# Kernel optimization log

Hardware: AMD Instinct MI355X
Metric: run time of the kernel (lower is better)

The kernel has to match this reference:

```python
import jax, jax.numpy as jnp
import numpy as np

BATCH, SEQ, D_IN, D_OUT = 32, 1024, 128, 128
NEG_SLOPE = 0.1


def setup_inputs() -> dict:
    key = jax.random.key(0)
    k1, k2, k3, k4 = jax.random.split(key, 4)
    nodes = jax.random.normal(k1, (BATCH, SEQ, D_IN), dtype=jnp.float32)
    adjacent = jax.random.randint(k2, (BATCH, SEQ, SEQ), 0, 2, dtype=jnp.int32)
    W = jax.random.normal(k3, (D_IN, D_OUT), dtype=jnp.float32) / np.sqrt(D_IN)
    B = jax.random.normal(k4, (D_IN, D_OUT), dtype=jnp.float32) / np.sqrt(D_IN)
    return {"nodes": nodes, "adjacent": adjacent, "W": W, "B": B}


def reference(nodes, adjacent, W, B):
    # mask[b, out, in] = 1 if edge (out -> in) present
    mask = (adjacent != 0).astype(nodes.dtype)
    # counts[b, in] = in-degree (number of 'out' neighbors pooled per target node)
    counts = mask.sum(axis=1)                               # [b, s_in]
    # segment-sum of neighbor features: pooled[b, in, d] = sum_out mask * nodes[b, out, d]
    pooled = jnp.einsum('boi,bod->bid', mask, nodes)        # [b, s_in, d]
    # mean over neighbors; nodes with zero degree get no pooled contribution
    pooled = jnp.where(counts[..., None] > 0,
                       pooled / jnp.maximum(counts, 1.0)[..., None],
                       jnp.zeros((), dtype=nodes.dtype))
    updated = nodes @ B + pooled @ W                        # [b, s, d_out]
    return jax.nn.leaky_relu(updated, negative_slope=NEG_SLOPE)
```

## Files before the change

### kernel.cpp

```cpp
#include <hip/hip_runtime.h>
#include <hip/hip_bf16.h>

#define SEQ 1024
#define DIM 128
#define NEG_SLOPE 0.1f

typedef __bf16 bf16x8 __attribute__((ext_vector_type(8)));
typedef float f32x4v __attribute__((ext_vector_type(4)));
typedef int   i32x4  __attribute__((ext_vector_type(4)));

#define BUF_STRIDE 32768
#define NODES_OFF  16384

__device__ __forceinline__ int fxv(int x) {
    return ((x & 3) | ((x & 1) << 2)) ^ ((x >> 2) & 7);
}
__device__ __forceinline__ int swz(int row, int unit) {
    return row * 128 + ((unit ^ fxv(row >> 2)) << 4);
}
__device__ __forceinline__ int swz256(int row, int unit) {
    return row * 256 + ((unit ^ fxv(row >> 2)) << 4);
}
__device__ __forceinline__ void bar() {
    asm volatile("s_waitcnt lgkmcnt(0)" ::: "memory");
    __builtin_amdgcn_s_barrier();
    __builtin_amdgcn_sched_barrier(0);
}
__device__ __forceinline__ unsigned short bfb(float f) {
    __bf16 h = (__bf16)f;
    return __builtin_bit_cast(unsigned short, h);
}
__device__ __forceinline__ unsigned bpack(float a, float b) {
    return (unsigned)bfb(a) | ((unsigned)bfb(b) << 16);
}
__device__ __forceinline__ unsigned mpack(int x0, int x1) {
    unsigned m0 = (x0 != 0) ? 0x3F80u : 0u;
    unsigned m1 = (x1 != 0) ? 0x3F80u : 0u;
    return m0 | (m1 << 16);
}

__global__ __launch_bounds__(512, 1)
void gcn_fused(const float* __restrict__ nodes,
               const int* __restrict__ adj,
               const float* __restrict__ W,
               const float* __restrict__ Bm,
               float* __restrict__ out)
{
    __shared__ alignas(16) unsigned char lds[2 * BUF_STRIDE];

    const int bid   = blockIdx.x;
    const int xcd   = bid & 7;
    const int slot  = bid >> 3;
    const int batch = ((slot >> 3) << 3) | xcd;
    const int itile = slot & 7;
    const int i0    = itile << 7;

    const int tid  = threadIdx.x;
    const int wave = tid >> 6;
    const int lane = tid & 63;
    const int wm   = wave >> 1;
    const int wn   = wave & 1;
    const int lrow = lane & 15;
    const int quad = lane >> 4;

    const int*   __restrict__ adj_b   = adj   + (size_t)batch * SEQ * SEQ;
    const float* __restrict__ nodes_b = nodes + (size_t)batch * SEQ * DIM;

    const int a_row = (tid >> 5) * 4;
    const int a_col = (tid & 31) * 4;
    const int n_col = (tid & 31) * 4;
    const int unit_s = (tid >> 5) >> 1;
    const int sub_s  = ((tid >> 5) & 1) * 8;

    f32x4v acc[2][4] = {};
    f32x4v acc_cnt[2] = {};
    bf16x8 ones;
    #pragma unroll
    for (int j = 0; j < 8; ++j) ones[j] = __builtin_bit_cast(__bf16, (unsigned short)0x3F80);

    i32x4  A0[4], A1[4];
    float4 N0[4], N1[4];

    auto load_chunk = [&](int o0, i32x4 (&A)[4], float4 (&N)[4]) {
        const int* pa = adj_b + (size_t)(o0 + a_row) * SEQ + (i0 + a_col);
        #pragma unroll
        for (int r = 0; r < 4; ++r)
            A[r] = __builtin_nontemporal_load((const i32x4*)(pa + (size_t)r * SEQ));
        const float* pn = nodes_b + (size_t)(o0 + a_row) * DIM + n_col;
        #pragma unroll
        for (int r = 0; r < 4; ++r) N[r] = *(const float4*)(pn + (size_t)r * DIM);
    };

    auto write_lds = [&](int base, const i32x4 (&A)[4], const float4 (&N)[4]) {
        unsigned char* mb = lds + base;
        unsigned char* nb = lds + base + NODES_OFF;
        #pragma unroll
        for (int j = 0; j < 4; ++j) {
            uint2 w;
            w.x = mpack(A[0][j], A[1][j]);
            w.y = mpack(A[2][j], A[3][j]);
            *(uint2*)(mb + swz(a_col + j, unit_s) + sub_s) = w;
        }
        #pragma unroll
        for (int j = 0; j < 4; ++j) {
            uint2 w;
            w.x = bpack(((const float*)&N[0])[j], ((const float*)&N[1])[j]);
            w.y = bpack(((const float*)&N[2])[j], ((const float*)&N[3])[j]);
            *(uint2*)(nb + swz(n_col + j, unit_s) + sub_s) = w;
        }
    };

    auto compute = [&](int base) {
        const unsigned char* mb = lds + base;
        const unsigned char* nb = lds + base + NODES_OFF;
        #pragma unroll
        for (int kk = 0; kk < 2; ++kk) {
            bf16x8 av[2], bv[4];
            #pragma unroll
            for (int mf = 0; mf < 2; ++mf)
                av[mf] = *(const bf16x8*)(mb + swz(wm * 32 + mf * 16 + lrow, 4 * kk + quad));
            #pragma unroll
            for (int nf = 0; nf < 4; ++nf)
                bv[nf] = *(const bf16x8*)(nb + swz(wn * 64 + nf * 16 + lrow, 4 * kk + quad));
            #pragma unroll
            for (int mf = 0; mf < 2; ++mf) {
                #pragma unroll
                for (int nf = 0; nf < 4; ++nf)
                    acc[mf][nf] = __builtin_amdgcn_mfma_f32_16x16x32_bf16(av[mf], bv[nf], acc[mf][nf], 0, 0, 0);
                acc_cnt[mf] = __builtin_amdgcn_mfma_f32_16x16x32_bf16(av[mf], ones, acc_cnt[mf], 0, 0, 0);
            }
        }
    };

    load_chunk(0,   A0, N0);
    load_chunk(64,  A1, N1);
    write_lds(0, A0, N0);
    load_chunk(128, A0, N0);
    bar();

    for (int cc = 0; cc < 8; ++cc) {
        const int c0 = cc * 2;
        compute(0);
        write_lds(BUF_STRIDE, A1, N1);
        if (c0 + 3 < 16) load_chunk((c0 + 3) * 64, A1, N1);
        bar();
        compute(BUF_STRIDE);
        if (c0 + 2 < 16) write_lds(0, A0, N0);
        if (c0 + 4 < 16) load_chunk((c0 + 4) * 64, A0, N0);
        bar();
    }


    #pragma unroll
    for (int mf = 0; mf < 2; ++mf) {
        #pragma unroll
        for (int r = 0; r < 4; ++r) {
            const int row = wm * 32 + mf * 16 + quad * 4 + r;
            const float cnt = acc_cnt[mf][r];
            const float inv = (cnt > 0.5f) ? 1.0f / cnt : 0.0f;
            #pragma unroll
            for (int nf = 0; nf < 4; ++nf) {
                const int col = wn * 64 + nf * 16 + lrow;
                *(unsigned short*)(lds + row * 256 + ((((col >> 3) ^ fxv(row >> 2)) << 4))
                                   + (col & 7) * 2) = bfb(acc[mf][nf][r] * inv);
            }
        }
    }

    const int n4 = (tid & 31) * 4;
    const int kg = tid >> 5;
    {
        float4 v[8];
        const float* pw = W + (size_t)(kg * 8) * DIM + n4;
        #pragma unroll
        for (int r = 0; r < 8; ++r) v[r] = *(const float4*)(pw + (size_t)r * DIM);
        #pragma unroll
        for (int j = 0; j < 4; ++j) {
            uint4 u;
            u.x = bpack(((const float*)&v[0])[j], ((const float*)&v[1])[j]);
            u.y = bpack(((const float*)&v[2])[j], ((const float*)&v[3])[j]);
            u.z = bpack(((const float*)&v[4])[j], ((const float*)&v[5])[j]);
            u.w = bpack(((const float*)&v[6])[j], ((const float*)&v[7])[j]);
            *(uint4*)(lds + BUF_STRIDE + swz256(n4 + j, kg)) = u;
        }
    }
    bar();

    f32x4v acc2[2][4] = {};

    #pragma unroll
    for (int ks = 0; ks < 4; ++ks) {
        const int un = ks * 4 + quad;
        bf16x8 av[2], bv[4];
        #pragma unroll
        for (int mf = 0; mf < 2; ++mf)
            av[mf] = *(const bf16x8*)(lds + swz256(wm * 32 + mf * 16 + lrow, un));
        #pragma unroll
        for (int nf = 0; nf < 4; ++nf)
            bv[nf] = *(const bf16x8*)(lds + BUF_STRIDE + swz256(wn * 64 + nf * 16 + lrow, un));
        #pragma unroll
        for (int mf = 0; mf < 2; ++mf)
            #pragma unroll
            for (int nf = 0; nf < 4; ++nf)
                acc2[mf][nf] = __builtin_amdgcn_mfma_f32_16x16x32_bf16(av[mf], bv[nf], acc2[mf][nf], 0, 0, 0);
    }
    bar();

    {
        float4 v[8];
        const float* pb = Bm + (size_t)(kg * 8) * DIM + n4;
        #pragma unroll
        for (int r = 0; r < 8; ++r) v[r] = *(const float4*)(pb + (size_t)r * DIM);
        #pragma unroll
        for (int j = 0; j < 4; ++j) {
            uint4 u;
            u.x = bpack(((const float*)&v[0])[j], ((const float*)&v[1])[j]);
            u.y = bpack(((const float*)&v[2])[j], ((const float*)&v[3])[j]);
            u.z = bpack(((const float*)&v[4])[j], ((const float*)&v[5])[j]);
            u.w = bpack(((const float*)&v[6])[j], ((const float*)&v[7])[j]);
            *(uint4*)(lds + swz256(n4 + j, kg)) = u;
        }
    }
    bar();

    #pragma unroll
    for (int ks = 0; ks < 4; ++ks) {
        const int k0 = ks * 32 + quad * 8;
        const int un = ks * 4 + quad;
        bf16x8 av[2], bv[4];
        #pragma unroll
        for (int mf = 0; mf < 2; ++mf) {
            const float* p = nodes_b + (size_t)(i0 + wm * 32 + mf * 16 + lrow) * DIM + k0;
            const float4 f1 = *(const float4*)p;
            const float4 f2 = *(const float4*)(p + 4);
            av[mf][0] = (__bf16)f1.x; av[mf][1] = (__bf16)f1.y;
            av[mf][2] = (__bf16)f1.z; av[mf][3] = (__bf16)f1.w;
            av[mf][4] = (__bf16)f2.x; av[mf][5] = (__bf16)f2.y;
            av[mf][6] = (__bf16)f2.z; av[mf][7] = (__bf16)f2.w;
        }
        #pragma unroll
        for (int nf = 0; nf < 4; ++nf)
            bv[nf] = *(const bf16x8*)(lds + swz256(wn * 64 + nf * 16 + lrow, un));
        #pragma unroll
        for (int mf = 0; mf < 2; ++mf)
            #pragma unroll
            for (int nf = 0; nf < 4; ++nf)
                acc2[mf][nf] = __builtin_amdgcn_mfma_f32_16x16x32_bf16(av[mf], bv[nf], acc2[mf][nf], 0, 0, 0);
    }

    float* out_b = out + (size_t)batch * SEQ * DIM;
    #pragma unroll
    for (int mf = 0; mf < 2; ++mf) {
        #pragma unroll
        for (int nf = 0; nf < 4; ++nf) {
            const int col = wn * 64 + nf * 16 + lrow;
            #pragma unroll
            for (int r = 0; r < 4; ++r) {
                const int row = i0 + wm * 32 + mf * 16 + quad * 4 + r;
                const float x = acc2[mf][nf][r];
                out_b[(size_t)row * DIM + col] = (x > 0.0f) ? x : NEG_SLOPE * x;
            }
        }
    }
}

extern "C" void kernel_launch(void* const* d_in, const int* in_sizes, int n_in,
                              void* d_out, int out_size, void* d_ws, size_t ws_size,
                              hipStream_t stream) {
    const float* nodes = (const float*)d_in[0];
    const int*   adj   = (const int*)d_in[1];
    const float* W     = (const float*)d_in[2];
    const float* Bm    = (const float*)d_in[3];
    float*       out   = (float*)d_out;
    gcn_fused<<<dim3(256), dim3(512), 0, stream>>>(nodes, adj, W, Bm, out);
}
```

Before: 214.5 us.

## Interleave LDS fragment loads, writes and MFMA clusters in ping-pong phases with setprio

Splits each double-buffered chunk step into four phases. In each phase one k-slice of fragments is read from LDS, half of the next chunk's mask or nodes data is written and its global loads are issued, then a barrier is followed by an MFMA cluster run at raised wave priority. The aim is to overlap LDS and global traffic with matrix work across waves and to spread register pressure. It doubles the number of barriers, and the bare s_barrier placement plus the synchronization ordering between the writes and later reads need care.

```diff
diff --git a/kernel.cpp b/kernel.cpp
--- a/kernel.cpp
+++ b/kernel.cpp
@@ -20,6 +20,13 @@
 }
 __device__ __forceinline__ int swz256(int row, int unit) {
     return row * 256 + ((unit ^ fxv(row >> 2)) << 4);
+}
+__device__ __forceinline__ void sbar() {
+    asm volatile("s_barrier" ::: "memory");
+}
+__device__ __forceinline__ void lgkm0() {
+    asm volatile("s_waitcnt lgkmcnt(0)" ::: "memory");
+    __builtin_amdgcn_sched_barrier(0);
 }
 __device__ __forceinline__ void bar() {
     asm volatile("s_waitcnt lgkmcnt(0)" ::: "memory");
@@ -81,19 +88,19 @@
     i32x4  A0[4], A1[4];
     float4 N0[4], N1[4];
 
-    auto load_chunk = [&](int o0, i32x4 (&A)[4], float4 (&N)[4]) {
+    auto load_adj = [&](int o0, i32x4 (&A)[4]) {
         const int* pa = adj_b + (size_t)(o0 + a_row) * SEQ + (i0 + a_col);
         #pragma unroll
         for (int r = 0; r < 4; ++r)
             A[r] = __builtin_nontemporal_load((const i32x4*)(pa + (size_t)r * SEQ));
+    };
+    auto load_nod = [&](int o0, float4 (&N)[4]) {
         const float* pn = nodes_b + (size_t)(o0 + a_row) * DIM + n_col;
         #pragma unroll
         for (int r = 0; r < 4; ++r) N[r] = *(const float4*)(pn + (size_t)r * DIM);
     };
-
-    auto write_lds = [&](int base, const i32x4 (&A)[4], const float4 (&N)[4]) {
+    auto write_mask = [&](int base, const i32x4 (&A)[4]) {
         unsigned char* mb = lds + base;
-        unsigned char* nb = lds + base + NODES_OFF;
         #pragma unroll
         for (int j = 0; j < 4; ++j) {
             uint2 w;
@@ -101,6 +108,9 @@
             w.y = mpack(A[2][j], A[3][j]);
             *(uint2*)(mb + swz(a_col + j, unit_s) + sub_s) = w;
         }
+    };
+    auto write_nod = [&](int base, const float4 (&N)[4]) {
+        unsigned char* nb = lds + base + NODES_OFF;
         #pragma unroll
         for (int j = 0; j < 4; ++j) {
             uint2 w;
@@ -109,47 +119,66 @@
             *(uint2*)(nb + swz(n_col + j, unit_s) + sub_s) = w;
         }
     };
-
-    auto compute = [&](int base) {
+    auto frags = [&](int base, int kk, bf16x8 (&av)[2], bf16x8 (&bv)[4]) {
         const unsigned char* mb = lds + base;
         const unsigned char* nb = lds + base + NODES_OFF;
         #pragma unroll
-        for (int kk = 0; kk < 2; ++kk) {
-            bf16x8 av[2], bv[4];
-            #pragma unroll
-            for (int mf = 0; mf < 2; ++mf)
-                av[mf] = *(const bf16x8*)(mb + swz(wm * 32 + mf * 16 + lrow, 4 * kk + quad));
+        for (int mf = 0; mf < 2; ++mf)
+            av[mf] = *(const bf16x8*)(mb + swz(wm * 32 + mf * 16 + lrow, 4 * kk + quad));
+        #pragma unroll
+        for (int nf = 0; nf < 4; ++nf)
+            bv[nf] = *(const bf16x8*)(nb + swz(wn * 64 + nf * 16 + lrow, 4 * kk + quad));
+    };
+    auto mfma_cluster = [&](const bf16x8 (&av)[2], const bf16x8 (&bv)[4]) {
+        __builtin_amdgcn_s_setprio(1);
+        #pragma unroll
+        for (int mf = 0; mf < 2; ++mf) {
             #pragma unroll
             for (int nf = 0; nf < 4; ++nf)
-                bv[nf] = *(const bf16x8*)(nb + swz(wn * 64 + nf * 16 + lrow, 4 * kk + quad));
-            #pragma unroll
-            for (int mf = 0; mf < 2; ++mf) {
-                #pragma unroll
-                for (int nf = 0; nf < 4; ++nf)
-                    acc[mf][nf] = __builtin_amdgcn_mfma_f32_16x16x32_bf16(av[mf], bv[nf], acc[mf][nf], 0, 0, 0);
-                acc_cnt[mf] = __builtin_amdgcn_mfma_f32_16x16x32_bf16(av[mf], ones, acc_cnt[mf], 0, 0, 0);
-            }
-        }
-    };
-
-    load_chunk(0,   A0, N0);
-    load_chunk(64,  A1, N1);
-    write_lds(0, A0, N0);
-    load_chunk(128, A0, N0);
+                acc[mf][nf] = __builtin_amdgcn_mfma_f32_16x16x32_bf16(av[mf], bv[nf], acc[mf][nf], 0, 0, 0);
+            acc_cnt[mf] = __builtin_amdgcn_mfma_f32_16x16x32_bf16(av[mf], ones, acc_cnt[mf], 0, 0, 0);
+        }
+        __builtin_amdgcn_s_setprio(0);
+    };
+
+    load_adj(0, A0);    load_nod(0, N0);
+    load_adj(64, A1);   load_nod(64, N1);
+    write_mask(0, A0);  write_nod(0, N0);
+    load_adj(128, A0);  load_nod(128, N0);
     bar();
 
     for (int cc = 0; cc < 8; ++cc) {
-        const int c0 = cc * 2;
-        compute(0);
-        write_lds(BUF_STRIDE, A1, N1);
-        if (c0 + 3 < 16) load_chunk((c0 + 3) * 64, A1, N1);
-        bar();
-        compute(BUF_STRIDE);
-        if (c0 + 2 < 16) write_lds(0, A0, N0);
-        if (c0 + 4 < 16) load_chunk((c0 + 4) * 64, A0, N0);
-        bar();
-    }
-
+        const int c0 = 2 * cc;
+        bf16x8 av[2], bv[4];
+
+        frags(0, 0, av, bv);
+        write_mask(BUF_STRIDE, A1);
+        if (c0 + 3 < 16) load_adj((c0 + 3) * 64, A1);
+        sbar(); lgkm0();
+        mfma_cluster(av, bv);
+        sbar();
+
+        frags(0, 1, av, bv);
+        write_nod(BUF_STRIDE, N1);
+        if (c0 + 3 < 16) load_nod((c0 + 3) * 64, N1);
+        sbar(); lgkm0();
+        mfma_cluster(av, bv);
+        sbar();
+
+        frags(BUF_STRIDE, 0, av, bv);
+        if (c0 + 2 < 16) write_mask(0, A0);
+        if (c0 + 4 < 16) load_adj((c0 + 4) * 64, A0);
+        sbar(); lgkm0();
+        mfma_cluster(av, bv);
+        sbar();
+
+        frags(BUF_STRIDE, 1, av, bv);
+        if (c0 + 2 < 16) write_nod(0, N0);
+        if (c0 + 4 < 16) load_nod((c0 + 4) * 64, N0);
+        sbar(); lgkm0();
+        mfma_cluster(av, bv);
+        sbar();
+    }
 
     #pragma unroll
     for (int mf = 0; mf < 2; ++mf) {
```

Result: no change. 213.6 us (-0.4%).
